# Performance work log

Hardware: AMD Instinct MI355X
Metric: run time of the kernel (lower is better)

The kernel has to match this reference:

```python
import jax, jax.numpy as jnp
import numpy as np
from jax import lax

D_MODEL = 512
D_STATE = 32
D_CONV = 4
D_INNER = 2 * D_MODEL
DT_RANK = (D_MODEL + 15) // 16  # 32
B_SZ, L = 8, 1024
EPS = 1e-12


def _mamba_params(key, pfx):
    ks = jax.random.split(key, 6)
    s = 0.02
    p = {}
    p[pfx + '_in_w'] = jax.random.normal(ks[0], (2 * D_INNER, D_MODEL)) * s
    p[pfx + '_conv_w'] = jax.random.normal(ks[1], (D_INNER, D_CONV)) * s
    p[pfx + '_conv_b'] = jnp.zeros((D_INNER,))
    p[pfx + '_xproj_w'] = jax.random.normal(ks[2], (DT_RANK + 2 * D_STATE, D_INNER)) * s
    p[pfx + '_dt_w'] = jax.random.normal(ks[3], (D_INNER, DT_RANK)) * s
    p[pfx + '_dt_b'] = jax.random.uniform(ks[4], (D_INNER,), minval=-4.0, maxval=-2.0)
    p[pfx + '_A_log'] = jnp.log(jnp.broadcast_to(jnp.arange(1, D_STATE + 1, dtype=jnp.float32), (D_INNER, D_STATE)))
    p[pfx + '_D'] = jnp.ones((D_INNER,))
    p[pfx + '_out_w'] = jax.random.normal(ks[5], (D_MODEL, D_INNER)) * s
    return p


def setup_inputs() -> dict:
    key = jax.random.key(0)
    ks = jax.random.split(key, 10)
    inp = {
        'hidden_states': jax.random.normal(ks[0], (B_SZ, L, D_MODEL)),
        'lengths': jax.random.randint(ks[1], (B_SZ,), 1, L + 1, dtype=jnp.int32),
    }
    inp.update(_mamba_params(ks[2], 'f'))
    inp.update(_mamba_params(ks[3], 'b'))
    s = 0.02
    inp['proj_w'] = jax.random.normal(ks[4], (1, 2)) * 0.5 + 0.5
    inp['proj_b'] = jnp.zeros((1,))
    inp['ln_g'] = jnp.ones((D_MODEL,))
    inp['ln_b'] = jnp.zeros((D_MODEL,))
    inp['ffn_w1'] = jax.random.normal(ks[5], (4 * D_MODEL, D_MODEL)) * s
    inp['ffn_b1'] = jnp.zeros((4 * D_MODEL,))
    inp['ffn_w2'] = jax.random.normal(ks[6], (D_MODEL, 4 * D_MODEL)) * s
    inp['ffn_b2'] = jnp.zeros((D_MODEL,))
    inp['ffn_ln_g'] = jnp.ones((D_MODEL,))
    inp['ffn_ln_b'] = jnp.zeros((D_MODEL,))
    return inp


def _layernorm(x, g, b):
    mu = jnp.mean(x, -1, keepdims=True)
    var = jnp.mean(jnp.square(x - mu), -1, keepdims=True)
    return (x - mu) * lax.rsqrt(var + EPS) * g + b


def _selective_scan(delta, Bm, Cm, u, A, D):
    # delta,u: (B,L,Di); Bm,Cm: (B,L,N); A: (Di,N); D: (Di,)
    def step(h, inp):
        d_t, B_t, C_t, u_t = inp
        dA = jnp.exp(d_t[..., None] * A)                 # (B,Di,N)
        h = dA * h + (d_t * u_t)[..., None] * B_t[:, None, :]
        y = jnp.einsum('bdn,bn->bd', h, C_t)
        return h, y
    h0 = jnp.zeros((u.shape[0], A.shape[0], A.shape[1]), u.dtype)
    xs = (delta.transpose(1, 0, 2), Bm.transpose(1, 0, 2),
          Cm.transpose(1, 0, 2), u.transpose(1, 0, 2))
    _, ys = lax.scan(step, h0, xs)
    return ys.transpose(1, 0, 2) + u * D


def _mamba(x, in_w, conv_w, conv_b, xproj_w, dt_w, dt_b, A_log, Dp, out_w):
    xz = jnp.einsum('bld,ed->ble', x, in_w)              # (B,L,2Di)
    x_in, z = jnp.split(xz, 2, axis=-1)
    # causal depthwise conv1d
    xc = jnp.pad(x_in.transpose(0, 2, 1), ((0, 0), (0, 0), (D_CONV - 1, 0)))
    xc = lax.conv_general_dilated(xc, conv_w[:, None, :], (1,), 'VALID',
                                  dimension_numbers=('NCH', 'OIH', 'NCH'),
                                  feature_group_count=D_INNER)
    xc = jax.nn.silu(xc + conv_b[None, :, None]).transpose(0, 2, 1)  # (B,L,Di)
    x_dbl = jnp.einsum('bld,ed->ble', xc, xproj_w)
    dt, Bm, Cm = jnp.split(x_dbl, [DT_RANK, DT_RANK + D_STATE], axis=-1)
    delta = jax.nn.softplus(jnp.einsum('blr,dr->bld', dt, dt_w) + dt_b)
    A = -jnp.exp(A_log)
    y = _selective_scan(delta, Bm, Cm, xc, A, Dp)
    y = y * jax.nn.silu(z)
    return jnp.einsum('bld,ed->ble', y, out_w)


def reference(hidden_states, lengths,
              f_in_w, f_conv_w, f_conv_b, f_xproj_w, f_dt_w, f_dt_b, f_A_log, f_D, f_out_w,
              b_in_w, b_conv_w, b_conv_b, b_xproj_w, b_dt_w, b_dt_b, b_A_log, b_D, b_out_w,
              proj_w, proj_b, ln_g, ln_b,
              ffn_w1, ffn_b1, ffn_w2, ffn_b2, ffn_ln_g, ffn_ln_b):
    x = hidden_states
    hf = _mamba(x, f_in_w, f_conv_w, f_conv_b, f_xproj_w, f_dt_w, f_dt_b, f_A_log, f_D, f_out_w)
    hb = _mamba(jnp.flip(x, 1), b_in_w, b_conv_w, b_conv_b, b_xproj_w, b_dt_w, b_dt_b, b_A_log, b_D, b_out_w)
    hb = jnp.flip(hb, 1)
    # Linear(2,1) over stacked [hf,hb] on last axis
    out = hf * proj_w[0, 0] + hb * proj_w[0, 1] + proj_b[0]
    out1 = _layernorm(out + x, ln_g, ln_b)  # dropout = identity (eval)
    h = jax.nn.gelu(jnp.einsum('bld,ed->ble', out1, ffn_w1) + ffn_b1, approximate=False)
    h = jnp.einsum('ble,de->bld', h, ffn_w2) + ffn_b2
    return _layernorm(h + out1, ffn_ln_g, ffn_ln_b)
```

## Files before the change

### kernel.cpp

```cpp
#include <hip/hip_runtime.h>
#include <hip/hip_bf16.h>
#include <hip/hip_fp16.h>
#include <math.h>

typedef __hip_bfloat16 bf16;
typedef __attribute__((ext_vector_type(8))) short bfrag;
typedef __attribute__((ext_vector_type(4))) float ffrag;
typedef __attribute__((ext_vector_type(4))) float f4;
typedef __attribute__((ext_vector_type(4))) short sh4;

#define BSZ    8
#define LSEQ   1024
#define DMODEL 512
#define DINNER 1024
#define DSTATE 32
#define DTRANK 32
#define MROWS  (BSZ * LSEQ)

__device__ __forceinline__ float bf2f(bf16 v) { return __bfloat162float(v); }
__device__ __forceinline__ float s2f(short s) {
    union { unsigned u; float f; } c; c.u = ((unsigned)(unsigned short)s) << 16; return c.f;
}
__device__ __forceinline__ short f2s(float v) {
    union { bf16 b; short s; } u; u.b = __float2bfloat16(v); return u.s;
}
__device__ __forceinline__ void stC(float* p, size_t i, float v) { p[i] = v; }
__device__ __forceinline__ void stC(bf16* p, size_t i, float v) { p[i] = __float2bfloat16(v); }
__device__ __forceinline__ float fsigmoid(float x) {
    return __builtin_amdgcn_rcpf(1.f + __expf(-x));
}
__device__ __forceinline__ float fexp2(float x) { return __builtin_amdgcn_exp2f(x); }

__device__ __forceinline__ float dload(const void* p, size_t i, int f) {
    if (f == 1) return ((const float*)p)[i];
    if (f == 2) return __half2float(((const __half*)p)[i]);
    if (f == 3) return (float)((const double*)p)[i];
    return bf2f(((const bf16*)p)[i]);
}

enum { ACT_NONE = 0, ACT_SOFTPLUS = 1, ACT_GELU = 2 };

__global__ void resolve_kernel(const void* a8, const void* d9, const void* d22,
                               const void* s0, const void* s1, int* flags)
{
    if (threadIdx.x != 0 || blockIdx.x != 0) return;
    const int cand[4] = {1, 0, 2, 3};
    int fw = -1;
    for (int ci = 0; ci < 4 && fw < 0; ++ci) {
        int f = cand[ci];
        bool ok = true;
        for (int k = 0; k < 48 && ok; ++k) {
            float e = logf((float)((k & 31) + 1));
            float v = dload(a8, k, f);
            ok = (v == v) && fabsf(v - e) <= 0.02f * e + 0.02f;
        }
        for (int k = 0; k < 8 && ok; ++k)
            ok = fabsf(dload(d9, k, f) - 1.f) <= 0.01f &&
                 fabsf(dload(d22, k, f) - 1.f) <= 0.01f;
        if (ok) fw = f;
    }
    int fx = -1, xs = -1;
    for (int si = 0; si < 2 && fx < 0; ++si) {
        const void* p = (si == 0) ? s0 : s1;
        for (int ci = 0; ci < 4 && fx < 0; ++ci) {
            int f = cand[ci];
            bool ok = true;
            float s = 0.f, s2 = 0.f;
            for (int k = 0; k < 256 && ok; ++k) {
                float v = dload(p, k, f);
                ok = (v == v) && fabsf(v) < 16.f;
                s += v; s2 += v * v;
            }
            if (ok) {
                float mu = s * (1.f / 256.f);
                float var = s2 * (1.f / 256.f) - mu * mu;
                if (var > 0.25f && var < 4.f) { fx = f; xs = si; }
            }
        }
    }
    flags[0] = (fw < 0) ? 1 : fw;
    flags[1] = (fx < 0) ? 1 : fx;
    flags[2] = (xs < 0) ? 0 : xs;
    flags[3] = (fw == 1 && fx == 1) ? 1 : 0;
}

__global__ __launch_bounds__(256) void cvt_x_kernel(const void* x0, const void* x1,
                                                    bf16* __restrict__ dst,
                                                    const int* __restrict__ flags)
{
    const void* x = flags[2] ? x1 : x0;
    const int fx = flags[1];
    int i = blockIdx.x * 256 + threadIdx.x;
    if (fx == 1) {
        f4 v = ((const f4*)x)[i];
        sh4 o;
#pragma unroll
        for (int j = 0; j < 4; ++j) o[j] = f2s(v[j]);
        ((sh4*)dst)[i] = o;
    } else {
#pragma unroll
        for (int j = 0; j < 4; ++j)
            dst[(size_t)i * 4 + j] = __float2bfloat16(dload(x, (size_t)i * 4 + j, fx));
    }
}

__global__ __launch_bounds__(256) void cvt_w_kernel(const float* __restrict__ src,
                                                    bf16* __restrict__ dst, int n4)
{
    int i = blockIdx.x * 256 + threadIdx.x;
    if (i >= n4) return;
    f4 v = ((const f4*)src)[i];
    sh4 o;
#pragma unroll
    for (int j = 0; j < 4; ++j) o[j] = f2s(v[j]);
    ((sh4*)dst)[i] = o;
}

__global__ __launch_bounds__(256) void transpose_kernel(
    const bf16* __restrict__ src, bf16* __restrict__ dst, int R, int D)
{
    __shared__ short t[64][72];
    const int r0 = blockIdx.x * 64, d0 = blockIdx.y * 64;
    const int tr = threadIdx.x >> 3;
    const int tc = (threadIdx.x & 7) * 8;
#pragma unroll
    for (int h = 0; h < 2; ++h) {
        int d = tr + h * 32;
        bfrag v = *(const bfrag*)&src[(size_t)(d0 + d) * R + r0 + tc];
#pragma unroll
        for (int j = 0; j < 8; ++j) t[tc + j][d] = v[j];
    }
    __syncthreads();
#pragma unroll
    for (int h = 0; h < 2; ++h) {
        int r = tr + h * 32;
        bfrag v = *(const bfrag*)&t[r][tc];
        *(bfrag*)&dst[(size_t)(r0 + r) * D + d0 + tc] = v;
    }
}

__device__ __forceinline__ void glds16(const bf16* g, short* l)
{
    __builtin_amdgcn_global_load_lds(
        (const __attribute__((address_space(1))) void*)g,
        (__attribute__((address_space(3))) void*)l,
        16, 0, 0);
}

template <int FLIPB, int ACT, typename CT>
__global__ __launch_bounds__(256) void bgemm_kernel(
    const bf16* __restrict__ A, int lda,
    const bf16* __restrict__ B, int ldb,
    const float* __restrict__ bias,
    CT* __restrict__ C, int ldc, int K)
{
    __shared__ __align__(16) short As[128 * 32];
    __shared__ __align__(16) short Bs[128 * 32];
    const int tid = threadIdx.x;
    const int bm = blockIdx.y * 128, bn = blockIdx.x * 128;
    const int lane = tid & 63, w = tid >> 6;

    const int srow = lane >> 2;
    const int skc  = (lane & 3) << 3;
    const int arow0 = bm + w * 32 + srow;
    int brow0 = bn + w * 32 + srow;
    int brow1 = brow0 + 16;
    if (FLIPB) {
        brow0 = (brow0 & ~(LSEQ - 1)) + (LSEQ - 1 - (brow0 & (LSEQ - 1)));
        brow1 = (brow1 & ~(LSEQ - 1)) + (LSEQ - 1 - (brow1 & (LSEQ - 1)));
    }
    const bf16* ga0 = A + (size_t)arow0 * lda + skc;
    const bf16* ga1 = ga0 + (size_t)16 * lda;
    const bf16* gb0 = B + (size_t)brow0 * ldb + skc;
    const bf16* gb1 = B + (size_t)brow1 * ldb + skc;
    short* la0 = &As[(w * 32) * 32];
    short* la1 = &As[(w * 32 + 16) * 32];
    short* lb0 = &Bs[(w * 32) * 32];
    short* lb1 = &Bs[(w * 32 + 16) * 32];

    const int wm = (w & 1) << 6, wn = (w >> 1) << 6;
    const int lm = lane & 15, quad = lane >> 4;

    ffrag acc[4][4];
#pragma unroll
    for (int i = 0; i < 4; ++i)
#pragma unroll
        for (int j = 0; j < 4; ++j)
#pragma unroll
            for (int e = 0; e < 4; ++e) acc[i][j][e] = 0.f;

    for (int k0 = 0; k0 < K; k0 += 32) {
        glds16(ga0 + k0, la0);
        glds16(ga1 + k0, la1);
        glds16(gb0 + k0, lb0);
        glds16(gb1 + k0, lb1);
        __syncthreads();
        bfrag af[4], bfv[4];
#pragma unroll
        for (int ti = 0; ti < 4; ++ti)
            af[ti] = *(const bfrag*)&As[(wm + ti * 16 + lm) * 32 + quad * 8];
#pragma unroll
        for (int tj = 0; tj < 4; ++tj)
            bfv[tj] = *(const bfrag*)&Bs[(wn + tj * 16 + lm) * 32 + quad * 8];
#pragma unroll
        for (int ti = 0; ti < 4; ++ti)
#pragma unroll
            for (int tj = 0; tj < 4; ++tj)
                acc[ti][tj] = __builtin_amdgcn_mfma_f32_16x16x32_bf16(
                    af[ti], bfv[tj], acc[ti][tj], 0, 0, 0);
        __syncthreads();
    }

#pragma unroll
    for (int tj = 0; tj < 4; ++tj) {
        int col = bn + wn + tj * 16 + lm;
        float bcv = bias ? bias[col] : 0.f;
#pragma unroll
        for (int ti = 0; ti < 4; ++ti) {
#pragma unroll
            for (int r2 = 0; r2 < 4; ++r2) {
                int rowg = bm + wm + ti * 16 + quad * 4 + r2;
                float v = acc[ti][tj][r2] + bcv;
                if (ACT == ACT_GELU) v = 0.5f * v * (1.f + erff(v * 0.70710678118654752f));
                stC(C, (size_t)rowg * ldc + col, v);
            }
        }
    }
}

template <int GUARD, int ACT, typename CT>
__global__ __launch_bounds__(256) void bgemm64_kernel(
    const bf16* __restrict__ A, int lda,
    const bf16* __restrict__ B, int ldb,
    const float* __restrict__ bias,
    CT* __restrict__ C, int ldc, int N, int K)
{
    __shared__ __align__(16) short As[128 * 32];
    __shared__ __align__(16) short Bs[64 * 32];
    const int tid = threadIdx.x;
    const int bm = blockIdx.y * 128, bn = blockIdx.x * 64;
    const int lane = tid & 63, w = tid >> 6;

    const int srow = lane >> 2;
    const int skc  = (lane & 3) << 3;
    const int arow0 = bm + w * 32 + srow;
    int brow = bn + w * 16 + srow;
    if (GUARD) brow = min(brow, N - 1);
    const bf16* ga0 = A + (size_t)arow0 * lda + skc;
    const bf16* ga1 = ga0 + (size_t)16 * lda;
    const bf16* gb0 = B + (size_t)brow * ldb + skc;
    short* la0 = &As[(w * 32) * 32];
    short* la1 = &As[(w * 32 + 16) * 32];
    short* lb0 = &Bs[(w * 16) * 32];

    const int wm = (w & 1) << 6, wn = (w >> 1) << 5;
    const int lm = lane & 15, quad = lane >> 4;

    ffrag acc[4][2];
#pragma unroll
    for (int i = 0; i < 4; ++i)
#pragma unroll
        for (int j = 0; j < 2; ++j)
#pragma unroll
            for (int e = 0; e < 4; ++e) acc[i][j][e] = 0.f;

    for (int k0 = 0; k0 < K; k0 += 32) {
        glds16(ga0 + k0, la0);
        glds16(ga1 + k0, la1);
        glds16(gb0 + k0, lb0);
        __syncthreads();
        bfrag af[4], bfv[2];
#pragma unroll
        for (int ti = 0; ti < 4; ++ti)
            af[ti] = *(const bfrag*)&As[(wm + ti * 16 + lm) * 32 + quad * 8];
#pragma unroll
        for (int tj = 0; tj < 2; ++tj)
            bfv[tj] = *(const bfrag*)&Bs[(wn + tj * 16 + lm) * 32 + quad * 8];
#pragma unroll
        for (int ti = 0; ti < 4; ++ti)
#pragma unroll
            for (int tj = 0; tj < 2; ++tj)
                acc[ti][tj] = __builtin_amdgcn_mfma_f32_16x16x32_bf16(
                    af[ti], bfv[tj], acc[ti][tj], 0, 0, 0);
        __syncthreads();
    }

#pragma unroll
    for (int tj = 0; tj < 2; ++tj) {
        int col = bn + wn + tj * 16 + lm;
        if (!GUARD || col < N) {
            float bcv = bias ? bias[col] : 0.f;
#pragma unroll
            for (int ti = 0; ti < 4; ++ti) {
#pragma unroll
                for (int r2 = 0; r2 < 4; ++r2) {
                    int rowg = bm + wm + ti * 16 + quad * 4 + r2;
                    float v = acc[ti][tj][r2] + bcv;
                    if (ACT == ACT_GELU) v = 0.5f * v * (1.f + erff(v * 0.70710678118654752f));
                    stC(C, (size_t)rowg * ldc + col, v);
                }
            }
        }
    }
}

template <int AM, int WHID, int FLIPW, int ACT, int BROW, typename CT>
__global__ __launch_bounds__(256) void mgemm_kernel(
    const void* __restrict__ A, int lda,
    const void* __restrict__ W0, const void* __restrict__ W1, int ldw,
    const float* __restrict__ bias,
    CT* __restrict__ C, int ldc, int M, int N, int K,
    const int* __restrict__ flags)
{
    __shared__ short As[128 * 40];
    __shared__ short Ws[128 * 40];
    const int tid = threadIdx.x;
    const int bm = blockIdx.y * 128;
    const int bn = blockIdx.x * 128;
    const float* Wp = (const float*)(WHID ? (flags[2] ? W1 : W0) : W0);

    const int r = tid >> 1;
    const int hcol = (tid & 1) << 4;
    int wrow = bn + r;
    if (FLIPW) { int b = wrow >> 10, l = wrow & 1023; wrow = (b << 10) + (1023 - l); }

    const int lane = tid & 63, w = tid >> 6;
    const int wm = (w & 1) << 6, wn = (w >> 1) << 6;
    const int lm = lane & 15, quad = lane >> 4;

    ffrag acc[4][4];
#pragma unroll
    for (int i = 0; i < 4; ++i)
#pragma unroll
        for (int j = 0; j < 4; ++j)
#pragma unroll
            for (int e = 0; e < 4; ++e) acc[i][j][e] = 0.f;

    for (int k0 = 0; k0 < K; k0 += 32) {
        if (AM == 2) {
            int kk = tid >> 3;
            int mc = tid & 7;
            const bf16* src = (const bf16*)A + (size_t)(k0 + kk) * lda + bm + mc * 16;
            bfrag v0 = *(const bfrag*)src;
            bfrag v1 = *(const bfrag*)(src + 8);
#pragma unroll
            for (int i = 0; i < 8; ++i) {
                As[(mc * 16 + i) * 40 + kk] = v0[i];
                As[(mc * 16 + 8 + i) * 40 + kk] = v1[i];
            }
        } else if (AM == 0) {
            const bf16* src = (const bf16*)A + (size_t)(bm + r) * lda + k0 + hcol;
            *(bfrag*)&As[r * 40 + hcol] = *(const bfrag*)src;
            *(bfrag*)&As[r * 40 + hcol + 8] = *(const bfrag*)(src + 8);
        } else {
            const float* src = (const float*)A + (size_t)(bm + r) * lda + k0 + hcol;
            float t[16];
            ((f4*)t)[0] = ((const f4*)src)[0];
            ((f4*)t)[1] = ((const f4*)src)[1];
            ((f4*)t)[2] = ((const f4*)src)[2];
            ((f4*)t)[3] = ((const f4*)src)[3];
            bfrag s0, s1;
#pragma unroll
            for (int i = 0; i < 8; ++i) { s0[i] = f2s(t[i]); s1[i] = f2s(t[8 + i]); }
            *(bfrag*)&As[r * 40 + hcol] = s0;
            *(bfrag*)&As[r * 40 + hcol + 8] = s1;
        }
        {
            bfrag s0, s1;
            if (bn + r < N) {
                const float* src = Wp + (size_t)wrow * ldw + k0 + hcol;
                float t[16];
                ((f4*)t)[0] = ((const f4*)src)[0];
                ((f4*)t)[1] = ((const f4*)src)[1];
                ((f4*)t)[2] = ((const f4*)src)[2];
                ((f4*)t)[3] = ((const f4*)src)[3];
#pragma unroll
                for (int i = 0; i < 8; ++i) { s0[i] = f2s(t[i]); s1[i] = f2s(t[8 + i]); }
            } else {
#pragma unroll
                for (int i = 0; i < 8; ++i) { s0[i] = 0; s1[i] = 0; }
            }
            *(bfrag*)&Ws[r * 40 + hcol] = s0;
            *(bfrag*)&Ws[r * 40 + hcol + 8] = s1;
        }
        __syncthreads();

        bfrag af[4], bfv[4];
#pragma unroll
        for (int ti = 0; ti < 4; ++ti)
            af[ti] = *(const bfrag*)&As[(wm + ti * 16 + lm) * 40 + quad * 8];
#pragma unroll
        for (int tj = 0; tj < 4; ++tj)
            bfv[tj] = *(const bfrag*)&Ws[(wn + tj * 16 + lm) * 40 + quad * 8];
#pragma unroll
        for (int ti = 0; ti < 4; ++ti)
#pragma unroll
            for (int tj = 0; tj < 4; ++tj)
                acc[ti][tj] = __builtin_amdgcn_mfma_f32_16x16x32_bf16(
                    af[ti], bfv[tj], acc[ti][tj], 0, 0, 0);
        __syncthreads();
    }

#pragma unroll
    for (int tj = 0; tj < 4; ++tj) {
        int col = bn + wn + tj * 16 + lm;
        if (col < N) {
            float bcv = (bias && !BROW) ? bias[col] : 0.f;
#pragma unroll
            for (int ti = 0; ti < 4; ++ti) {
#pragma unroll
                for (int r2 = 0; r2 < 4; ++r2) {
                    int rowg = bm + wm + ti * 16 + quad * 4 + r2;
                    float v = acc[ti][tj][r2] + bcv;
                    if (BROW && bias) v += bias[rowg];
                    if (ACT == ACT_SOFTPLUS) v = (v > 20.f) ? v : log1pf(expf(v));
                    else if (ACT == ACT_GELU) v = 0.5f * v * (1.f + erff(v * 0.70710678118654752f));
                    stC(C, (size_t)rowg * ldc + col, v);
                }
            }
        }
    }
}

__global__ __launch_bounds__(256) void conv_silu_kernel(
    const bf16* __restrict__ xin_T,
    const void* __restrict__ cw,
    const void* __restrict__ cb,
    bf16* __restrict__ u_T,
    const int* __restrict__ flags)
{
    const int fw = flags[0];
    int blk = blockIdx.x;
    int chunk = blk & 3;
    int db = blk >> 2;
    int b = db & 7;
    int d = db >> 3;
    int l = chunk * 256 + threadIdx.x;
    size_t base = (size_t)d * MROWS + b * LSEQ;
    float w0 = dload(cw, d * 4 + 0, fw), w1 = dload(cw, d * 4 + 1, fw);
    float w2 = dload(cw, d * 4 + 2, fw), w3 = dload(cw, d * 4 + 3, fw);
    float acc = dload(cb, d, fw);
    if (l >= 3) acc += bf2f(xin_T[base + l - 3]) * w0;
    if (l >= 2) acc += bf2f(xin_T[base + l - 2]) * w1;
    if (l >= 1) acc += bf2f(xin_T[base + l - 1]) * w2;
    acc += bf2f(xin_T[base + l]) * w3;
    u_T[base + l] = __float2bfloat16(acc * fsigmoid(acc));
}

#define SCH 8
struct ScanBuf { float dl[SCH], uv[SCH], Bv[SCH], Cv[SCH]; float zsc, usc; };

__device__ __forceinline__ void scan_load(ScanBuf& s,
    const bf16* __restrict__ dT, const bf16* __restrict__ uT,
    const bf16* __restrict__ zT, const float* __restrict__ xdbl,
    size_t lb, size_t mb, int n)
{
    bfrag dv = *(const bfrag*)&dT[lb];
    bfrag uv = *(const bfrag*)&uT[lb];
#pragma unroll
    for (int j = 0; j < SCH; ++j) { s.dl[j] = s2f(dv[j]); s.uv[j] = s2f(uv[j]); }
    s.zsc = bf2f(zT[lb + (n & 7)]);
    s.usc = bf2f(uT[lb + (n & 7)]);
#pragma unroll
    for (int j = 0; j < SCH; ++j) {
        s.Bv[j] = xdbl[(mb + j) * 96 + 32 + n];
        s.Cv[j] = xdbl[(mb + j) * 96 + 64 + n];
    }
}

__device__ __forceinline__ void scan_compute(const ScanBuf& s, float& h,
    float Ad2, float Dd, bf16* __restrict__ yT, size_t lb,
    bool b0, bool b1, bool b2, bool wr)
{
    float p[SCH];
#pragma unroll
    for (int j = 0; j < SCH; ++j) {
        float dlv = s.dl[j];
        h = fexp2(dlv * Ad2) * h + dlv * s.uv[j] * s.Bv[j];
        p[j] = h * s.Cv[j];
    }
    float q[4];
#pragma unroll
    for (int jj = 0; jj < 4; ++jj) {
        float keep = b0 ? p[2 * jj + 1] : p[2 * jj];
        float send = b0 ? p[2 * jj] : p[2 * jj + 1];
        q[jj] = keep + __shfl_xor(send, 1);
    }
    float r0 = (b1 ? q[1] : q[0]) + __shfl_xor(b1 ? q[0] : q[1], 2);
    float r1 = (b1 ? q[3] : q[2]) + __shfl_xor(b1 ? q[2] : q[3], 2);
    float t = (b2 ? r1 : r0) + __shfl_xor(b2 ? r0 : r1, 4);
    t += __shfl_xor(t, 8);
    t += __shfl_xor(t, 16);
    if (wr) {
        float y = t + s.usc * Dd;
        float g = s.zsc;
        y *= g * fsigmoid(g);
        yT[lb + (threadIdx.x & 7)] = __float2bfloat16(y);
    }
}

__global__ __launch_bounds__(256) void scan_kernel(
    const bf16* __restrict__ delta_T,
    bf16* __restrict__ u_T,
    const bf16* __restrict__ z_T,
    const float* __restrict__ xdbl,
    const void* __restrict__ A_log,
    const void* __restrict__ Dp,
    const int* __restrict__ flags)
{
    const int fw = flags[0];
    const int tid = threadIdx.x;
    const int n = tid & 31;
    const int dloc = tid >> 5;
    const int gd = blockIdx.x * 8 + dloc;
    const int b = gd >> 10;
    const int d = gd & (DINNER - 1);
    const bool b0 = n & 1, b1 = n & 2, b2 = n & 4;
    const bool wr = (n < 8);

    const float Ad2 = -__expf(dload(A_log, d * DSTATE + n, fw)) * 1.44269504088896341f;
    const float Dd = dload(Dp, d, fw);
    const size_t lbase = (size_t)d * MROWS + b * LSEQ;
    const size_t mbase = (size_t)b * LSEQ;
    float h = 0.f;

    ScanBuf bufA, bufB;
    scan_load(bufA, delta_T, u_T, z_T, xdbl, lbase, mbase, n);
    for (int c0 = 0; c0 < LSEQ / SCH; c0 += 2) {
        scan_load(bufB, delta_T, u_T, z_T, xdbl,
                  lbase + (size_t)(c0 + 1) * SCH, mbase + (size_t)(c0 + 1) * SCH, n);
        scan_compute(bufA, h, Ad2, Dd, u_T, lbase + (size_t)c0 * SCH, b0, b1, b2, wr);
        if (c0 + 2 < LSEQ / SCH)
            scan_load(bufA, delta_T, u_T, z_T, xdbl,
                      lbase + (size_t)(c0 + 2) * SCH, mbase + (size_t)(c0 + 2) * SCH, n);
        scan_compute(bufB, h, Ad2, Dd, u_T, lbase + (size_t)(c0 + 1) * SCH, b0, b1, b2, wr);
    }
}

__global__ __launch_bounds__(256) void combine_ln_kernel(
    const bf16* __restrict__ hf, const bf16* __restrict__ hb,
    const void* __restrict__ x0, const void* __restrict__ x1,
    const void* __restrict__ pw, const void* __restrict__ pb,
    const void* __restrict__ g, const void* __restrict__ be,
    bf16* __restrict__ out1,
    const int* __restrict__ flags)
{
    const int fw = flags[0];
    const int fx = flags[1];
    const void* x = flags[2] ? x1 : x0;
    int row = blockIdx.x;
    int b = row >> 10, l = row & (LSEQ - 1);
    int rrow = (b << 10) + (LSEQ - 1 - l);
    float pw0 = dload(pw, 0, fw), pw1 = dload(pw, 1, fw), pbv = dload(pb, 0, fw);
    __shared__ float red[2][4];
    float v[2], s = 0.f, s2 = 0.f;
#pragma unroll
    for (int i = 0; i < 2; ++i) {
        int c = threadIdx.x + i * 256;
        float val = bf2f(hf[(size_t)row * DMODEL + c]) * pw0
                  + bf2f(hb[(size_t)rrow * DMODEL + c]) * pw1
                  + pbv + dload(x, (size_t)row * DMODEL + c, fx);
        v[i] = val; s += val; s2 += val * val;
    }
    for (int m = 1; m < 64; m <<= 1) { s += __shfl_xor(s, m); s2 += __shfl_xor(s2, m); }
    int w = threadIdx.x >> 6;
    if ((threadIdx.x & 63) == 0) { red[0][w] = s; red[1][w] = s2; }
    __syncthreads();
    s = red[0][0] + red[0][1] + red[0][2] + red[0][3];
    s2 = red[1][0] + red[1][1] + red[1][2] + red[1][3];
    float mu = s * (1.f / DMODEL);
    float var = s2 * (1.f / DMODEL) - mu * mu;
    float r = rsqrtf(fmaxf(var, 0.f) + 1e-12f);
#pragma unroll
    for (int i = 0; i < 2; ++i) {
        int c = threadIdx.x + i * 256;
        float val = (v[i] - mu) * r * dload(g, c, fw) + dload(be, c, fw);
        out1[(size_t)row * DMODEL + c] = __float2bfloat16(val);
    }
}

__global__ __launch_bounds__(256) void final_ln_kernel(
    const float* __restrict__ out2, const bf16* __restrict__ out1,
    const void* __restrict__ g, const void* __restrict__ be,
    float* __restrict__ out,
    const int* __restrict__ flags)
{
    const int fw = flags[0];
    const int valid = flags[3];
    int row = blockIdx.x;
    __shared__ float red[2][4];
    float v[2], s = 0.f, s2 = 0.f;
#pragma unroll
    for (int i = 0; i < 2; ++i) {
        int c = threadIdx.x + i * 256;
        float val = out2[(size_t)row * DMODEL + c] + bf2f(out1[(size_t)row * DMODEL + c]);
        v[i] = val; s += val; s2 += val * val;
    }
    for (int m = 1; m < 64; m <<= 1) { s += __shfl_xor(s, m); s2 += __shfl_xor(s2, m); }
    int w = threadIdx.x >> 6;
    if ((threadIdx.x & 63) == 0) { red[0][w] = s; red[1][w] = s2; }
    __syncthreads();
    s = red[0][0] + red[0][1] + red[0][2] + red[0][3];
    s2 = red[1][0] + red[1][1] + red[1][2] + red[1][3];
    float mu = s * (1.f / DMODEL);
    float var = s2 * (1.f / DMODEL) - mu * mu;
    float r = rsqrtf(fmaxf(var, 0.f) + 1e-12f);
#pragma unroll
    for (int i = 0; i < 2; ++i) {
        int c = threadIdx.x + i * 256;
        float val = (v[i] - mu) * r * dload(g, c, fw) + dload(be, c, fw);
        out[(size_t)row * DMODEL + c] = valid ? val : 0.f;
    }
}

extern "C" void kernel_launch(void* const* d_in, const int* in_sizes, int n_in,
                              void* d_out, int out_size, void* d_ws, size_t ws_size,
                              hipStream_t stream)
{
    const void* x0 = d_in[0];
    const void* x1 = d_in[1];
    const void* proj_w   = d_in[20];
    const void* proj_b   = d_in[21];
    const void* ln_g     = d_in[22];
    const void* ln_b     = d_in[23];
    const float* ffn_w1  = (const float*)d_in[24];
    const float* ffn_b1  = (const float*)d_in[25];
    const float* ffn_w2  = (const float*)d_in[26];
    const float* ffn_b2  = (const float*)d_in[27];
    const void* ffn_ln_g = d_in[28];
    const void* ffn_ln_b = d_in[29];

    char* wsb = (char*)d_ws;
    char* ob  = (char*)d_out;
    bf16*  xin_T   = (bf16*)(wsb + 0);
    bf16*  z_T     = (bf16*)(wsb + (16u << 20));
    bf16*  uy_T    = (bf16*)(wsb + (32u << 20));
    bf16*  u_rm    = (bf16*)(wsb + 0);
    bf16*  delta_T = (bf16*)(wsb + 0);
    bf16*  y_rm    = (bf16*)(wsb + 0);
    float* xdbl    = (float*)(wsb + (48u << 20));
    bf16*  in_w_bf = (bf16*)(wsb + (51u << 20));
    bf16*  xp_w_bf = (bf16*)(wsb + (53u << 20));
    bf16*  o_w_bf  = (bf16*)(wsb + (54u << 20));
    bf16*  hf      = (bf16*)d_out;
    bf16*  hb      = (bf16*)d_out + (size_t)MROWS * DMODEL;
    bf16*  xbf     = (bf16*)(ob + (8u << 20));
    bf16*  w1bf    = (bf16*)(ob + 0);
    bf16*  w2bf    = (bf16*)(ob + (2u << 20));
    bf16*  out1    = (bf16*)(wsb + 0);
    bf16*  ffn_h   = (bf16*)(wsb + (8u << 20));
    float* out2    = (float*)(wsb + (40u << 20));
    int*   flags   = (int*)(wsb + (56u << 20));

    dim3 blk(256);

    resolve_kernel<<<dim3(1), dim3(64), 0, stream>>>(
        d_in[8], d_in[9], d_in[22], x0, x1, flags);
    cvt_x_kernel<<<dim3(4096), blk, 0, stream>>>(x0, x1, xbf, flags);

    for (int dir = 0; dir < 2; ++dir) {
        int pb0 = 2 + dir * 9;
        const float* in_w    = (const float*)d_in[pb0 + 0];
        const void*  conv_w  = d_in[pb0 + 1];
        const void*  conv_b  = d_in[pb0 + 2];
        const float* xproj_w = (const float*)d_in[pb0 + 3];
        const float* dt_w    = (const float*)d_in[pb0 + 4];
        const float* dt_b    = (const float*)d_in[pb0 + 5];
        const void*  A_log   = d_in[pb0 + 6];
        const void*  Dp      = d_in[pb0 + 7];
        const float* out_w   = (const float*)d_in[pb0 + 8];
        bf16* hout = (dir == 0) ? hf : hb;

        cvt_w_kernel<<<dim3(1024), blk, 0, stream>>>(in_w, in_w_bf, (2048 * 512) / 4);
        cvt_w_kernel<<<dim3(96), blk, 0, stream>>>(xproj_w, xp_w_bf, (96 * 1024) / 4);
        cvt_w_kernel<<<dim3(512), blk, 0, stream>>>(out_w, o_w_bf, (512 * 1024) / 4);

        if (dir == 0)
            bgemm_kernel<0, ACT_NONE, bf16><<<dim3(64, 16), blk, 0, stream>>>(
                in_w_bf, DMODEL, xbf, DMODEL, nullptr, xin_T, MROWS, DMODEL);
        else
            bgemm_kernel<1, ACT_NONE, bf16><<<dim3(64, 16), blk, 0, stream>>>(
                in_w_bf, DMODEL, xbf, DMODEL, nullptr, xin_T, MROWS, DMODEL);

        conv_silu_kernel<<<dim3(DINNER * BSZ * 4), blk, 0, stream>>>(
            xin_T, conv_w, conv_b, uy_T, flags);
        transpose_kernel<<<dim3(128, 16), blk, 0, stream>>>(uy_T, u_rm, MROWS, DINNER);
        bgemm64_kernel<1, ACT_NONE, float><<<dim3(2, 64), blk, 0, stream>>>(
            u_rm, DINNER, xp_w_bf, DINNER, nullptr, xdbl, 96, 96, DINNER);
        mgemm_kernel<1, 0, 0, ACT_SOFTPLUS, 1, bf16><<<dim3(64, 8), blk, 0, stream>>>(
            dt_w, DTRANK, xdbl, nullptr, 96, dt_b,
            delta_T, MROWS, DINNER, MROWS, DTRANK, flags);
        scan_kernel<<<dim3((BSZ * DINNER) / 8), blk, 0, stream>>>(
            delta_T, uy_T, z_T, xdbl, A_log, Dp, flags);
        transpose_kernel<<<dim3(128, 16), blk, 0, stream>>>(uy_T, y_rm, MROWS, DINNER);
        bgemm64_kernel<0, ACT_NONE, bf16><<<dim3(8, 64), blk, 0, stream>>>(
            y_rm, DINNER, o_w_bf, DINNER, nullptr, hout, DMODEL, DMODEL, DINNER);
    }

    combine_ln_kernel<<<dim3(MROWS), blk, 0, stream>>>(
        hf, hb, x0, x1, proj_w, proj_b, ln_g, ln_b, out1, flags);
    cvt_w_kernel<<<dim3(1024), blk, 0, stream>>>(ffn_w1, w1bf, (2048 * 512) / 4);
    cvt_w_kernel<<<dim3(1024), blk, 0, stream>>>(ffn_w2, w2bf, (512 * 2048) / 4);
    bgemm_kernel<0, ACT_GELU, bf16><<<dim3(16, 64), blk, 0, stream>>>(
        out1, DMODEL, w1bf, DMODEL, ffn_b1, ffn_h, 2048, DMODEL);
    bgemm64_kernel<0, ACT_NONE, float><<<dim3(8, 64), blk, 0, stream>>>(
        ffn_h, 2048, w2bf, 2048, ffn_b2, out2, DMODEL, DMODEL, 2048);
    final_ln_kernel<<<dim3(MROWS), blk, 0, stream>>>(
        out2, out1, ffn_ln_g, ffn_ln_b, (float*)d_out, flags);
}
```

Measured before the change: 906.5 us.

## Transpose x_proj output, add dedicated dt kernel, widen bgemm64 K-tile with swizzle

The x_proj GEMM now computes a transposed output (96 x M), so the scan reads its B and C coefficients as contiguous vectors. The generic mgemm used for dt_proj plus softplus is replaced by a simple per-element dt_kernel with FMA loops. bgemm64 now stages a 64-wide K tile per iteration with an XOR-swizzled shared-memory layout to reduce bank conflicts and halve the barrier count, and guards rows instead of columns. The weight conversion launches are merged into one cvt3 kernel to cut launch overhead.

```diff
diff --git a/kernel.cpp b/kernel.cpp
--- a/kernel.cpp
+++ b/kernel.cpp
@@ -104,16 +104,22 @@
     }
 }
 
-__global__ __launch_bounds__(256) void cvt_w_kernel(const float* __restrict__ src,
-                                                    bf16* __restrict__ dst, int n4)
+__global__ __launch_bounds__(256) void cvt3_kernel(
+    const float* __restrict__ s0, bf16* __restrict__ d0, int n0,
+    const float* __restrict__ s1, bf16* __restrict__ d1, int n1,
+    const float* __restrict__ s2, bf16* __restrict__ d2, int n2)
 {
     int i = blockIdx.x * 256 + threadIdx.x;
-    if (i >= n4) return;
-    f4 v = ((const f4*)src)[i];
+    const float* s; bf16* d; int off;
+    if (i < n0) { s = s0; d = d0; off = i; }
+    else if (i < n0 + n1) { s = s1; d = d1; off = i - n0; }
+    else if (i < n0 + n1 + n2) { s = s2; d = d2; off = i - n0 - n1; }
+    else return;
+    f4 v = ((const f4*)s)[off];
     sh4 o;
 #pragma unroll
     for (int j = 0; j < 4; ++j) o[j] = f2s(v[j]);
-    ((sh4*)dst)[i] = o;
+    ((sh4*)d)[off] = o;
 }
 
 __global__ __launch_bounds__(256) void transpose_kernel(
@@ -228,30 +234,37 @@
     }
 }
 
-template <int GUARD, int ACT, typename CT>
+template <int ACT, typename CT>
 __global__ __launch_bounds__(256) void bgemm64_kernel(
     const bf16* __restrict__ A, int lda,
     const bf16* __restrict__ B, int ldb,
     const float* __restrict__ bias,
-    CT* __restrict__ C, int ldc, int N, int K)
-{
-    __shared__ __align__(16) short As[128 * 32];
-    __shared__ __align__(16) short Bs[64 * 32];
+    CT* __restrict__ C, int ldc, int M, int K)
+{
+    __shared__ __align__(16) short As[128 * 64];
+    __shared__ __align__(16) short Bs[64 * 64];
     const int tid = threadIdx.x;
     const int bm = blockIdx.y * 128, bn = blockIdx.x * 64;
     const int lane = tid & 63, w = tid >> 6;
 
-    const int srow = lane >> 2;
-    const int skc  = (lane & 3) << 3;
-    const int arow0 = bm + w * 32 + srow;
-    int brow = bn + w * 16 + srow;
-    if (GUARD) brow = min(brow, N - 1);
-    const bf16* ga0 = A + (size_t)arow0 * lda + skc;
-    const bf16* ga1 = ga0 + (size_t)16 * lda;
-    const bf16* gb0 = B + (size_t)brow * ldb + skc;
-    short* la0 = &As[(w * 32) * 32];
-    short* la1 = &As[(w * 32 + 16) * 32];
-    short* lb0 = &Bs[(w * 16) * 32];
+    const int lr = lane >> 3;
+    const int sc = ((lane & 7) ^ lr) << 3;
+
+    const bf16* ga[4];
+#pragma unroll
+    for (int a = 0; a < 4; ++a) {
+        int ar = bm + w * 32 + a * 8 + lr;
+        if (ar >= M) ar = M - 1;
+        ga[a] = A + (size_t)ar * lda + sc;
+    }
+    const bf16* gb[2];
+#pragma unroll
+    for (int a = 0; a < 2; ++a) {
+        int br = bn + w * 16 + a * 8 + lr;
+        gb[a] = B + (size_t)br * ldb + sc;
+    }
+    short* la = &As[(w * 32) * 64];
+    short* lb = &Bs[(w * 16) * 64];
 
     const int wm = (w & 1) << 6, wn = (w >> 1) << 5;
     const int lm = lane & 15, quad = lane >> 4;
@@ -264,37 +277,49 @@
 #pragma unroll
             for (int e = 0; e < 4; ++e) acc[i][j][e] = 0.f;
 
-    for (int k0 = 0; k0 < K; k0 += 32) {
-        glds16(ga0 + k0, la0);
-        glds16(ga1 + k0, la1);
-        glds16(gb0 + k0, lb0);
+    for (int k0 = 0; k0 < K; k0 += 64) {
+#pragma unroll
+        for (int a = 0; a < 4; ++a) glds16(ga[a] + k0, la + a * 8 * 64);
+#pragma unroll
+        for (int a = 0; a < 2; ++a) glds16(gb[a] + k0, lb + a * 8 * 64);
         __syncthreads();
-        bfrag af[4], bfv[2];
-#pragma unroll
-        for (int ti = 0; ti < 4; ++ti)
-            af[ti] = *(const bfrag*)&As[(wm + ti * 16 + lm) * 32 + quad * 8];
-#pragma unroll
-        for (int tj = 0; tj < 2; ++tj)
-            bfv[tj] = *(const bfrag*)&Bs[(wn + tj * 16 + lm) * 32 + quad * 8];
-#pragma unroll
-        for (int ti = 0; ti < 4; ++ti)
-#pragma unroll
-            for (int tj = 0; tj < 2; ++tj)
-                acc[ti][tj] = __builtin_amdgcn_mfma_f32_16x16x32_bf16(
-                    af[ti], bfv[tj], acc[ti][tj], 0, 0, 0);
+        bfrag af[2][4], bfv[2][2];
+#pragma unroll
+        for (int kk = 0; kk < 2; ++kk) {
+#pragma unroll
+            for (int ti = 0; ti < 4; ++ti) {
+                int row = wm + ti * 16 + lm;
+                int c = kk * 4 + quad;
+                af[kk][ti] = *(const bfrag*)&As[row * 64 + ((c ^ (row & 7)) << 3)];
+            }
+#pragma unroll
+            for (int tj = 0; tj < 2; ++tj) {
+                int row = wn + tj * 16 + lm;
+                int c = kk * 4 + quad;
+                bfv[kk][tj] = *(const bfrag*)&Bs[row * 64 + ((c ^ (row & 7)) << 3)];
+            }
+        }
+#pragma unroll
+        for (int kk = 0; kk < 2; ++kk)
+#pragma unroll
+            for (int ti = 0; ti < 4; ++ti)
+#pragma unroll
+                for (int tj = 0; tj < 2; ++tj)
+                    acc[ti][tj] = __builtin_amdgcn_mfma_f32_16x16x32_bf16(
+                        af[kk][ti], bfv[kk][tj], acc[ti][tj], 0, 0, 0);
         __syncthreads();
     }
 
 #pragma unroll
     for (int tj = 0; tj < 2; ++tj) {
         int col = bn + wn + tj * 16 + lm;
-        if (!GUARD || col < N) {
-            float bcv = bias ? bias[col] : 0.f;
-#pragma unroll
-            for (int ti = 0; ti < 4; ++ti) {
-#pragma unroll
-                for (int r2 = 0; r2 < 4; ++r2) {
-                    int rowg = bm + wm + ti * 16 + quad * 4 + r2;
+        float bcv = bias ? bias[col] : 0.f;
+#pragma unroll
+        for (int ti = 0; ti < 4; ++ti) {
+#pragma unroll
+            for (int r2 = 0; r2 < 4; ++r2) {
+                int rowg = bm + wm + ti * 16 + quad * 4 + r2;
+                if (rowg < M) {
                     float v = acc[ti][tj][r2] + bcv;
                     if (ACT == ACT_GELU) v = 0.5f * v * (1.f + erff(v * 0.70710678118654752f));
                     stC(C, (size_t)rowg * ldc + col, v);
@@ -304,121 +329,23 @@
     }
 }
 
-template <int AM, int WHID, int FLIPW, int ACT, int BROW, typename CT>
-__global__ __launch_bounds__(256) void mgemm_kernel(
-    const void* __restrict__ A, int lda,
-    const void* __restrict__ W0, const void* __restrict__ W1, int ldw,
-    const float* __restrict__ bias,
-    CT* __restrict__ C, int ldc, int M, int N, int K,
-    const int* __restrict__ flags)
-{
-    __shared__ short As[128 * 40];
-    __shared__ short Ws[128 * 40];
-    const int tid = threadIdx.x;
-    const int bm = blockIdx.y * 128;
-    const int bn = blockIdx.x * 128;
-    const float* Wp = (const float*)(WHID ? (flags[2] ? W1 : W0) : W0);
-
-    const int r = tid >> 1;
-    const int hcol = (tid & 1) << 4;
-    int wrow = bn + r;
-    if (FLIPW) { int b = wrow >> 10, l = wrow & 1023; wrow = (b << 10) + (1023 - l); }
-
-    const int lane = tid & 63, w = tid >> 6;
-    const int wm = (w & 1) << 6, wn = (w >> 1) << 6;
-    const int lm = lane & 15, quad = lane >> 4;
-
-    ffrag acc[4][4];
-#pragma unroll
-    for (int i = 0; i < 4; ++i)
-#pragma unroll
-        for (int j = 0; j < 4; ++j)
-#pragma unroll
-            for (int e = 0; e < 4; ++e) acc[i][j][e] = 0.f;
-
-    for (int k0 = 0; k0 < K; k0 += 32) {
-        if (AM == 2) {
-            int kk = tid >> 3;
-            int mc = tid & 7;
-            const bf16* src = (const bf16*)A + (size_t)(k0 + kk) * lda + bm + mc * 16;
-            bfrag v0 = *(const bfrag*)src;
-            bfrag v1 = *(const bfrag*)(src + 8);
-#pragma unroll
-            for (int i = 0; i < 8; ++i) {
-                As[(mc * 16 + i) * 40 + kk] = v0[i];
-                As[(mc * 16 + 8 + i) * 40 + kk] = v1[i];
-            }
-        } else if (AM == 0) {
-            const bf16* src = (const bf16*)A + (size_t)(bm + r) * lda + k0 + hcol;
-            *(bfrag*)&As[r * 40 + hcol] = *(const bfrag*)src;
-            *(bfrag*)&As[r * 40 + hcol + 8] = *(const bfrag*)(src + 8);
-        } else {
-            const float* src = (const float*)A + (size_t)(bm + r) * lda + k0 + hcol;
-            float t[16];
-            ((f4*)t)[0] = ((const f4*)src)[0];
-            ((f4*)t)[1] = ((const f4*)src)[1];
-            ((f4*)t)[2] = ((const f4*)src)[2];
-            ((f4*)t)[3] = ((const f4*)src)[3];
-            bfrag s0, s1;
-#pragma unroll
-            for (int i = 0; i < 8; ++i) { s0[i] = f2s(t[i]); s1[i] = f2s(t[8 + i]); }
-            *(bfrag*)&As[r * 40 + hcol] = s0;
-            *(bfrag*)&As[r * 40 + hcol + 8] = s1;
-        }
-        {
-            bfrag s0, s1;
-            if (bn + r < N) {
-                const float* src = Wp + (size_t)wrow * ldw + k0 + hcol;
-                float t[16];
-                ((f4*)t)[0] = ((const f4*)src)[0];
-                ((f4*)t)[1] = ((const f4*)src)[1];
-                ((f4*)t)[2] = ((const f4*)src)[2];
-                ((f4*)t)[3] = ((const f4*)src)[3];
-#pragma unroll
-                for (int i = 0; i < 8; ++i) { s0[i] = f2s(t[i]); s1[i] = f2s(t[8 + i]); }
-            } else {
-#pragma unroll
-                for (int i = 0; i < 8; ++i) { s0[i] = 0; s1[i] = 0; }
-            }
-            *(bfrag*)&Ws[r * 40 + hcol] = s0;
-            *(bfrag*)&Ws[r * 40 + hcol + 8] = s1;
-        }
-        __syncthreads();
-
-        bfrag af[4], bfv[4];
-#pragma unroll
-        for (int ti = 0; ti < 4; ++ti)
-            af[ti] = *(const bfrag*)&As[(wm + ti * 16 + lm) * 40 + quad * 8];
-#pragma unroll
-        for (int tj = 0; tj < 4; ++tj)
-            bfv[tj] = *(const bfrag*)&Ws[(wn + tj * 16 + lm) * 40 + quad * 8];
-#pragma unroll
-        for (int ti = 0; ti < 4; ++ti)
-#pragma unroll
-            for (int tj = 0; tj < 4; ++tj)
-                acc[ti][tj] = __builtin_amdgcn_mfma_f32_16x16x32_bf16(
-                    af[ti], bfv[tj], acc[ti][tj], 0, 0, 0);
-        __syncthreads();
-    }
-
-#pragma unroll
-    for (int tj = 0; tj < 4; ++tj) {
-        int col = bn + wn + tj * 16 + lm;
-        if (col < N) {
-            float bcv = (bias && !BROW) ? bias[col] : 0.f;
-#pragma unroll
-            for (int ti = 0; ti < 4; ++ti) {
-#pragma unroll
-                for (int r2 = 0; r2 < 4; ++r2) {
-                    int rowg = bm + wm + ti * 16 + quad * 4 + r2;
-                    float v = acc[ti][tj][r2] + bcv;
-                    if (BROW && bias) v += bias[rowg];
-                    if (ACT == ACT_SOFTPLUS) v = (v > 20.f) ? v : log1pf(expf(v));
-                    else if (ACT == ACT_GELU) v = 0.5f * v * (1.f + erff(v * 0.70710678118654752f));
-                    stC(C, (size_t)rowg * ldc + col, v);
-                }
-            }
-        }
+__global__ __launch_bounds__(256) void dt_kernel(
+    const float* __restrict__ xdT,
+    const float* __restrict__ dt_w,
+    const float* __restrict__ dt_b,
+    bf16* __restrict__ delta_T)
+{
+    const int m = blockIdx.x * 256 + threadIdx.x;
+    const int d0 = blockIdx.y * 64;
+    float v[32];
+#pragma unroll
+    for (int r = 0; r < 32; ++r) v[r] = xdT[(size_t)r * MROWS + m];
+    for (int d = d0; d < d0 + 64; ++d) {
+        float acc = dt_b[d];
+#pragma unroll
+        for (int r = 0; r < 32; ++r) acc = fmaf(dt_w[d * 32 + r], v[r], acc);
+        acc = (acc > 20.f) ? acc : log1pf(__expf(acc));
+        delta_T[(size_t)d * MROWS + m] = __float2bfloat16(acc);
     }
 }
 
@@ -452,8 +379,8 @@
 
 __device__ __forceinline__ void scan_load(ScanBuf& s,
     const bf16* __restrict__ dT, const bf16* __restrict__ uT,
-    const bf16* __restrict__ zT, const float* __restrict__ xdbl,
-    size_t lb, size_t mb, int n)
+    const bf16* __restrict__ zT, const float* __restrict__ bB,
+    const float* __restrict__ bC, size_t lb, int t0, int n)
 {
     bfrag dv = *(const bfrag*)&dT[lb];
     bfrag uv = *(const bfrag*)&uT[lb];
@@ -461,10 +388,14 @@
     for (int j = 0; j < SCH; ++j) { s.dl[j] = s2f(dv[j]); s.uv[j] = s2f(uv[j]); }
     s.zsc = bf2f(zT[lb + (n & 7)]);
     s.usc = bf2f(uT[lb + (n & 7)]);
-#pragma unroll
-    for (int j = 0; j < SCH; ++j) {
-        s.Bv[j] = xdbl[(mb + j) * 96 + 32 + n];
-        s.Cv[j] = xdbl[(mb + j) * 96 + 64 + n];
+    f4 b0 = *(const f4*)&bB[t0];
+    f4 b1 = *(const f4*)&bB[t0 + 4];
+    f4 c0 = *(const f4*)&bC[t0];
+    f4 c1 = *(const f4*)&bC[t0 + 4];
+#pragma unroll
+    for (int j = 0; j < 4; ++j) {
+        s.Bv[j] = b0[j]; s.Bv[4 + j] = b1[j];
+        s.Cv[j] = c0[j]; s.Cv[4 + j] = c1[j];
     }
 }
 
@@ -503,7 +434,7 @@
     const bf16* __restrict__ delta_T,
     bf16* __restrict__ u_T,
     const bf16* __restrict__ z_T,
-    const float* __restrict__ xdbl,
+    const float* __restrict__ xdT,
     const void* __restrict__ A_log,
     const void* __restrict__ Dp,
     const int* __restrict__ flags)
@@ -521,18 +452,19 @@
     const float Ad2 = -__expf(dload(A_log, d * DSTATE + n, fw)) * 1.44269504088896341f;
     const float Dd = dload(Dp, d, fw);
     const size_t lbase = (size_t)d * MROWS + b * LSEQ;
-    const size_t mbase = (size_t)b * LSEQ;
+    const float* bB = xdT + (size_t)(32 + n) * MROWS + b * LSEQ;
+    const float* bC = xdT + (size_t)(64 + n) * MROWS + b * LSEQ;
     float h = 0.f;
 
     ScanBuf bufA, bufB;
-    scan_load(bufA, delta_T, u_T, z_T, xdbl, lbase, mbase, n);
+    scan_load(bufA, delta_T, u_T, z_T, bB, bC, lbase, 0, n);
     for (int c0 = 0; c0 < LSEQ / SCH; c0 += 2) {
-        scan_load(bufB, delta_T, u_T, z_T, xdbl,
-                  lbase + (size_t)(c0 + 1) * SCH, mbase + (size_t)(c0 + 1) * SCH, n);
+        scan_load(bufB, delta_T, u_T, z_T, bB, bC,
+                  lbase + (size_t)(c0 + 1) * SCH, (c0 + 1) * SCH, n);
         scan_compute(bufA, h, Ad2, Dd, u_T, lbase + (size_t)c0 * SCH, b0, b1, b2, wr);
         if (c0 + 2 < LSEQ / SCH)
-            scan_load(bufA, delta_T, u_T, z_T, xdbl,
-                      lbase + (size_t)(c0 + 2) * SCH, mbase + (size_t)(c0 + 2) * SCH, n);
+            scan_load(bufA, delta_T, u_T, z_T, bB, bC,
+                      lbase + (size_t)(c0 + 2) * SCH, (c0 + 2) * SCH, n);
         scan_compute(bufB, h, Ad2, Dd, u_T, lbase + (size_t)(c0 + 1) * SCH, b0, b1, b2, wr);
     }
 }
@@ -638,7 +570,7 @@
     bf16*  u_rm    = (bf16*)(wsb + 0);
     bf16*  delta_T = (bf16*)(wsb + 0);
     bf16*  y_rm    = (bf16*)(wsb + 0);
-    float* xdbl    = (float*)(wsb + (48u << 20));
+    float* xdT     = (float*)(wsb + (48u << 20));
     bf16*  in_w_bf = (bf16*)(wsb + (51u << 20));
     bf16*  xp_w_bf = (bf16*)(wsb + (53u << 20));
     bf16*  o_w_bf  = (bf16*)(wsb + (54u << 20));
@@ -671,9 +603,10 @@
         const float* out_w   = (const float*)d_in[pb0 + 8];
         bf16* hout = (dir == 0) ? hf : hb;
 
-        cvt_w_kernel<<<dim3(1024), blk, 0, stream>>>(in_w, in_w_bf, (2048 * 512) / 4);
-        cvt_w_kernel<<<dim3(96), blk, 0, stream>>>(xproj_w, xp_w_bf, (96 * 1024) / 4);
-        cvt_w_kernel<<<dim3(512), blk, 0, stream>>>(out_w, o_w_bf, (512 * 1024) / 4);
+        cvt3_kernel<<<dim3(1632), blk, 0, stream>>>(
+            in_w, in_w_bf, (2048 * 512) / 4,
+            xproj_w, xp_w_bf, (96 * 1024) / 4,
+            out_w, o_w_bf, (512 * 1024) / 4);
 
         if (dir == 0)
             bgemm_kernel<0, ACT_NONE, bf16><<<dim3(64, 16), blk, 0, stream>>>(
@@ -685,26 +618,26 @@
         conv_silu_kernel<<<dim3(DINNER * BSZ * 4), blk, 0, stream>>>(
             xin_T, conv_w, conv_b, uy_T, flags);
         transpose_kernel<<<dim3(128, 16), blk, 0, stream>>>(uy_T, u_rm, MROWS, DINNER);
-        bgemm64_kernel<1, ACT_NONE, float><<<dim3(2, 64), blk, 0, stream>>>(
-            u_rm, DINNER, xp_w_bf, DINNER, nullptr, xdbl, 96, 96, DINNER);
-        mgemm_kernel<1, 0, 0, ACT_SOFTPLUS, 1, bf16><<<dim3(64, 8), blk, 0, stream>>>(
-            dt_w, DTRANK, xdbl, nullptr, 96, dt_b,
-            delta_T, MROWS, DINNER, MROWS, DTRANK, flags);
+        bgemm64_kernel<ACT_NONE, float><<<dim3(128, 1), blk, 0, stream>>>(
+            xp_w_bf, DINNER, u_rm, DINNER, nullptr, xdT, MROWS, 96, DINNER);
+        dt_kernel<<<dim3(32, 16), blk, 0, stream>>>(xdT, dt_w, dt_b, delta_T);
         scan_kernel<<<dim3((BSZ * DINNER) / 8), blk, 0, stream>>>(
-            delta_T, uy_T, z_T, xdbl, A_log, Dp, flags);
+            delta_T, uy_T, z_T, xdT, A_log, Dp, flags);
         transpose_kernel<<<dim3(128, 16), blk, 0, stream>>>(uy_T, y_rm, MROWS, DINNER);
-        bgemm64_kernel<0, ACT_NONE, bf16><<<dim3(8, 64), blk, 0, stream>>>(
-            y_rm, DINNER, o_w_bf, DINNER, nullptr, hout, DMODEL, DMODEL, DINNER);
+        bgemm64_kernel<ACT_NONE, bf16><<<dim3(8, 64), blk, 0, stream>>>(
+            y_rm, DINNER, o_w_bf, DINNER, nullptr, hout, DMODEL, MROWS, DINNER);
     }
 
     combine_ln_kernel<<<dim3(MROWS), blk, 0, stream>>>(
         hf, hb, x0, x1, proj_w, proj_b, ln_g, ln_b, out1, flags);
-    cvt_w_kernel<<<dim3(1024), blk, 0, stream>>>(ffn_w1, w1bf, (2048 * 512) / 4);
-    cvt_w_kernel<<<dim3(1024), blk, 0, stream>>>(ffn_w2, w2bf, (512 * 2048) / 4);
+    cvt3_kernel<<<dim3(2048), blk, 0, stream>>>(
+        ffn_w1, w1bf, (2048 * 512) / 4,
+        ffn_w2, w2bf, (512 * 2048) / 4,
+        nullptr, nullptr, 0);
     bgemm_kernel<0, ACT_GELU, bf16><<<dim3(16, 64), blk, 0, stream>>>(
         out1, DMODEL, w1bf, DMODEL, ffn_b1, ffn_h, 2048, DMODEL);
-    bgemm64_kernel<0, ACT_NONE, float><<<dim3(8, 64), blk, 0, stream>>>(
-        ffn_h, 2048, w2bf, 2048, ffn_b2, out2, DMODEL, DMODEL, 2048);
+    bgemm64_kernel<ACT_NONE, float><<<dim3(8, 64), blk, 0, stream>>>(
+        ffn_h, 2048, w2bf, 2048, ffn_b2, out2, DMODEL, MROWS, 2048);
     final_ln_kernel<<<dim3(MROWS), blk, 0, stream>>>(
         out2, out1, ffn_ln_g, ffn_ln_b, (float*)d_out, flags);
 }
```

New measurement: 1.202 ms. +32.6%, slower.
